# Optimization experiments

Hardware: AMD Instinct MI355X
Metric: run time of the kernel (lower is better)

The kernel has to match this reference:

```python
import jax, jax.numpy as jnp
import numpy as np
import math

B, D, T, R = 32, 512, 64, 49
K = 64
OUT = 1024


def setup_inputs() -> dict:
    key = jax.random.key(0)
    k_x, k_c, k_w = jax.random.split(key, 3)
    x = jax.random.normal(k_x, (B, D, T, R), dtype=jnp.float32)
    mask = jnp.ones((B, T), dtype=jnp.int32)
    centroids = jax.random.normal(k_c, (K, D), dtype=jnp.float32) / math.sqrt(D)
    conv_w = centroids  # reset_parameters() copies centroids into the 1x1 conv weight
    red_w = jax.random.normal(k_w, (OUT, K * D), dtype=jnp.float32) / math.sqrt(K * D)
    ln_gamma = jnp.ones((OUT,), dtype=jnp.float32)
    ln_beta = jnp.zeros((OUT,), dtype=jnp.float32)
    return {"x": x, "mask": mask, "centroids": centroids, "conv_w": conv_w,
            "red_w": red_w, "ln_gamma": ln_gamma, "ln_beta": ln_beta}


def _l2norm(v, axis):
    n = jnp.sqrt(jnp.sum(v * v, axis=axis, keepdims=True))
    return v / jnp.maximum(n, 1e-12)


def reference(x, mask, centroids, conv_w, red_w, ln_gamma, ln_beta):
    b, d, t, r = x.shape
    # 1x1 conv == contraction over channel dim: [b,k,t,r]
    logits = jnp.einsum('bdtr,kd->bktr', x, conv_w)
    assign = jax.nn.softmax(logits, axis=1)
    # mask applied to residual*assign == masking the assignments
    m = mask.astype(x.dtype)[:, None, :, None]          # [b,1,t,1]
    assign = assign * m
    a_sum = jnp.sum(assign, axis=(2, 3))                 # [b,k]
    # vlad[b,k,d] = sum_{t,r} a[b,k,t,r]*x[b,d,t,r] - a_sum[b,k]*c[k,d]
    vlad = jnp.einsum('bktr,bdtr->bkd', assign, x) - a_sum[:, :, None] * centroids[None]
    vlad = _l2norm(vlad, axis=2)                         # intra-normalization
    vlad = vlad.reshape(b, -1)                           # [b, K*D]
    vlad = _l2norm(vlad, axis=1)
    vlad = vlad @ red_w.T                                # [b, OUT]
    # LayerNorm (eps=1e-5)
    mu = jnp.mean(vlad, axis=-1, keepdims=True)
    var = jnp.mean((vlad - mu) ** 2, axis=-1, keepdims=True)
    return (vlad - mu) / jnp.sqrt(var + 1e-5) * ln_gamma + ln_beta
```

## Files before the change

kernel.cpp:

```cpp
#include <hip/hip_runtime.h>
#include <math.h>

#define BB 32
#define DD 512
#define TT 64
#define RR 49
#define TR 3136
#define KK 64
#define OUTN 1024
#define KD 32768
#define PSTR 1048576ull

typedef float f4 __attribute__((ext_vector_type(4)));
typedef short s8 __attribute__((ext_vector_type(8)));

#define OFF_ASSIGN 0ull
#define OFF_VLADP  12845056ull
#define OFF_VN     29622272ull
#define OFF_CWB    31719424ull
#define OFF_SS     31784960ull
#define OFF_ASUM   31793152ull
#define OFF_Y      31801344ull

__device__ __forceinline__ unsigned long long pack4(float a, float b, float c, float d) {
    union { float f; unsigned u; } A, B, C, D;
    A.f = a; B.f = b; C.f = c; D.f = d;
    unsigned lo = __builtin_amdgcn_perm(B.u + 0x8000u, A.u + 0x8000u, 0x07060302u);
    unsigned hi = __builtin_amdgcn_perm(D.u + 0x8000u, C.u + 0x8000u, 0x07060302u);
    return (unsigned long long)lo | ((unsigned long long)hi << 32);
}

__global__ __launch_bounds__(256) void kW(const float* __restrict__ convw,
                                          unsigned short* __restrict__ cwb) {
    int idx = blockIdx.x * 256 + threadIdx.x;
    f4 v = *(const f4*)(convw + idx * 4);
    *(unsigned long long*)(cwb + idx * 4) = pack4(v[0], v[1], v[2], v[3]);
}

__global__ __launch_bounds__(256) void kA(const float* __restrict__ x,
                                          const int* __restrict__ mask,
                                          const unsigned short* __restrict__ cwb,
                                          unsigned short* __restrict__ assign,
                                          float* __restrict__ asum) {
    __shared__ unsigned short xT_l[64 * 136];
    __shared__ float sm[64 * 68];
    __shared__ float redM[256], redS[256];

    const int blk = blockIdx.x;
    const int b = blk / 49;
    const int pc = blk % 49;
    const int p0 = pc * 64;
    const int tid = threadIdx.x;
    const int lane = tid & 63;
    const int wv = tid >> 6;
    const int quad = lane >> 4;
    const int l15 = lane & 15;

    f4 acc[4];
#pragma unroll
    for (int t = 0; t < 4; ++t) acc[t] = (f4){0.f, 0.f, 0.f, 0.f};

    const float* xb = x + (size_t)b * DD * TR;
    const unsigned short* cwrow = cwb + (wv * 16 + l15) * DD + quad * 8;

    for (int dc = 0; dc < 4; ++dc) {
        const int d0 = dc * 128;
        s8 af[4];
#pragma unroll
        for (int ks = 0; ks < 4; ++ks) af[ks] = *(const s8*)(cwrow + d0 + ks * 32);
        __syncthreads();
#pragma unroll
        for (int i = 0; i < 2; ++i) {
            int lin = i * 256 + tid;
            int dq = lin >> 4;
            int pq = lin & 15;
            const float* xp = xb + (size_t)(d0 + dq * 4) * TR + p0 + pq * 4;
            f4 a0 = *(const f4*)(xp);
            f4 a1 = *(const f4*)(xp + TR);
            f4 a2 = *(const f4*)(xp + 2 * TR);
            f4 a3 = *(const f4*)(xp + 3 * TR);
#pragma unroll
            for (int jj = 0; jj < 4; ++jj) {
                int j = (jj + pq) & 3;
                *(unsigned long long*)(xT_l + (pq * 4 + j) * 136 + dq * 4) =
                    pack4(a0[j], a1[j], a2[j], a3[j]);
            }
        }
        __syncthreads();
#pragma unroll
        for (int ks = 0; ks < 4; ++ks) {
            int off = ks * 32 + quad * 8;
#pragma unroll
            for (int t = 0; t < 4; ++t) {
                s8 bfr = *(const s8*)(xT_l + (t * 16 + l15) * 136 + off);
                acc[t] = __builtin_amdgcn_mfma_f32_16x16x32_bf16(af[ks], bfr, acc[t], 0, 0, 0);
            }
        }
    }
#pragma unroll
    for (int t = 0; t < 4; ++t)
#pragma unroll
        for (int r = 0; r < 4; ++r)
            sm[(wv * 16 + quad * 4 + r) * 68 + t * 16 + l15] = acc[t][r];
    __syncthreads();

    const int p = lane;
    float mx = -1e30f;
#pragma unroll
    for (int i = 0; i < 16; ++i) mx = fmaxf(mx, sm[(wv * 16 + i) * 68 + p]);
    redM[wv * 64 + p] = mx;
    __syncthreads();
    mx = fmaxf(fmaxf(redM[p], redM[64 + p]), fmaxf(redM[128 + p], redM[192 + p]));
    float s = 0.f;
#pragma unroll
    for (int i = 0; i < 16; ++i) {
        float e = __expf(sm[(wv * 16 + i) * 68 + p] - mx);
        sm[(wv * 16 + i) * 68 + p] = e;
        s += e;
    }
    redS[wv * 64 + p] = s;
    __syncthreads();
    float tot = redS[p] + redS[64 + p] + redS[128 + p] + redS[192 + p];
    const int tt = (p0 + p) / RR;
    const float inv = (float)mask[b * TT + tt] / tot;
#pragma unroll
    for (int i = 0; i < 16; ++i) {
        float v = sm[(wv * 16 + i) * 68 + p] * inv;
        sm[(wv * 16 + i) * 68 + p] = v;
        float r = v;
#pragma unroll
        for (int off = 32; off > 0; off >>= 1) r += __shfl_down(r, off, 64);
        if (lane == 0) atomicAdd(&asum[b * 64 + wv * 16 + i], r);
    }
    __syncthreads();
#pragma unroll
    for (int i = 0; i < 4; ++i) {
        int lin = i * 256 + tid;
        int kr = lin >> 4;
        int pqq = lin & 15;
        f4 v = *(const f4*)(sm + kr * 68 + pqq * 4);
        *(unsigned long long*)(assign + (size_t)(b * 64 + kr) * TR + p0 + pqq * 4) =
            pack4(v[0], v[1], v[2], v[3]);
    }
}

__global__ __launch_bounds__(256) void kB(const float* __restrict__ x,
                                          const unsigned short* __restrict__ assign,
                                          const float* __restrict__ asum,
                                          const float* __restrict__ cent,
                                          float* __restrict__ vladP) {
    __shared__ unsigned short as_l[64 * 72];
    __shared__ unsigned short x_l[64 * 72];

    const int blk = blockIdx.x;
    const int b  = blk >> 5;
    const int ds = (blk >> 2) & 7;
    const int ph = blk & 3;
    const int d0 = ds * 64;
    const int tid = threadIdx.x;
    const int lane = tid & 63;
    const int wv = tid >> 6;
    const int quad = lane >> 4;
    const int l15 = lane & 15;

    f4 acc[4];
#pragma unroll
    for (int t = 0; t < 4; ++t) acc[t] = (f4){0.f, 0.f, 0.f, 0.f};

    const int pcs = (ph * 49) >> 2;
    const int pce = ((ph + 1) * 49) >> 2;

    const int ar0 = tid >> 3, ac0 = tid & 7;
    const int xr0 = tid >> 4, xc0 = tid & 15;

    s8 asr[2];
    f4 xrr[4];
    auto LOADB = [&](int pc) {
        const int pp = pc * 64;
#pragma unroll
        for (int i = 0; i < 2; ++i)
            asr[i] = *(const s8*)(assign + (size_t)(b * 64 + ar0 + i * 32) * TR + pp + ac0 * 8);
#pragma unroll
        for (int i = 0; i < 4; ++i)
            xrr[i] = *(const f4*)(x + (size_t)(b * DD + d0 + xr0 + i * 16) * TR + pp + xc0 * 4);
    };
    auto STOREB = [&]() {
#pragma unroll
        for (int i = 0; i < 2; ++i)
            *(s8*)(as_l + (ar0 + i * 32) * 72 + ac0 * 8) = asr[i];
#pragma unroll
        for (int i = 0; i < 4; ++i)
            *(unsigned long long*)(x_l + (xr0 + i * 16) * 72 + xc0 * 4) =
                pack4(xrr[i][0], xrr[i][1], xrr[i][2], xrr[i][3]);
    };

    LOADB(pcs);
    for (int pc = pcs; pc < pce; ++pc) {
        __syncthreads();
        STOREB();
        if (pc + 1 < pce) LOADB(pc + 1);
        __syncthreads();
#pragma unroll
        for (int ks = 0; ks < 2; ++ks) {
            const int off = ks * 32 + quad * 8;
            s8 af = *(const s8*)(as_l + (wv * 16 + l15) * 72 + off);
#pragma unroll
            for (int t = 0; t < 4; ++t) {
                s8 bfr = *(const s8*)(x_l + (t * 16 + l15) * 72 + off);
                acc[t] = __builtin_amdgcn_mfma_f32_16x16x32_bf16(af, bfr, acc[t], 0, 0, 0);
            }
        }
    }
    float* vp = vladP + (size_t)ph * PSTR;
#pragma unroll
    for (int r = 0; r < 4; ++r) {
        const int k = wv * 16 + quad * 4 + r;
        float corr = (ph == 0) ? asum[b * 64 + k] : 0.f;
#pragma unroll
        for (int t = 0; t < 4; ++t) {
            const int d = d0 + t * 16 + l15;
            float v = acc[t][r];
            if (ph == 0) v -= corr * cent[k * DD + d];
            vp[(size_t)(b * 64 + k) * DD + d] = v;
        }
    }
}

__global__ __launch_bounds__(256) void kC1(const float* __restrict__ vladP,
                                           float* __restrict__ ss) {
    const int blk = blockIdx.x;
    const int b = blk >> 3;
    const int ks = blk & 7;
    const int tid = threadIdx.x;
    const int kr = tid >> 5;
    const int l32 = tid & 31;
    const int k = ks * 8 + kr;
    const float* q = vladP + (size_t)(b * 64 + k) * DD;
    float s = 0.f;
#pragma unroll
    for (int i = 0; i < 4; ++i) {
        f4 a0 = *(const f4*)(q + i * 128 + l32 * 4);
        f4 a1 = *(const f4*)(q + PSTR + i * 128 + l32 * 4);
        f4 a2 = *(const f4*)(q + 2 * PSTR + i * 128 + l32 * 4);
        f4 a3 = *(const f4*)(q + 3 * PSTR + i * 128 + l32 * 4);
#pragma unroll
        for (int j = 0; j < 4; ++j) {
            float v = (a0[j] + a1[j]) + (a2[j] + a3[j]);
            s = fmaf(v, v, s);
        }
    }
    for (int off = 16; off > 0; off >>= 1) s += __shfl_down(s, off, 32);
    if (l32 == 0) ss[b * 64 + k] = s;
}

__global__ __launch_bounds__(256) void kC2(const float* __restrict__ vladP,
                                           const float* __restrict__ ss,
                                           unsigned short* __restrict__ vn) {
    __shared__ float sc[64];
    const int blk = blockIdx.x;
    const int b = blk >> 3;
    const int js = blk & 7;
    const int tid = threadIdx.x;
    if (tid < 64) {
        float rn = sqrtf(ss[b * 64 + tid]);
        float inv = 1.f / fmaxf(rn, 1e-12f);
        float cb = rn * inv; cb = cb * cb;
        float g = cb;
        for (int off = 32; off > 0; off >>= 1) g += __shfl_down(g, off, 64);
        g = __shfl(g, 0, 64);
        float gi = 1.f / fmaxf(sqrtf(g), 1e-12f);
        sc[tid] = inv * gi;
    }
    __syncthreads();
    const float* q = vladP + (size_t)b * KD;
#pragma unroll
    for (int it = 0; it < 4; ++it) {
        int j = js * 4096 + it * 1024 + tid * 4;
        f4 a0 = *(const f4*)(q + j);
        f4 a1 = *(const f4*)(q + PSTR + j);
        f4 a2 = *(const f4*)(q + 2 * PSTR + j);
        f4 a3 = *(const f4*)(q + 3 * PSTR + j);
        float scl = sc[j >> 9];
        *(unsigned long long*)(vn + (size_t)b * KD + j) =
            pack4(((a0[0] + a1[0]) + (a2[0] + a3[0])) * scl,
                  ((a0[1] + a1[1]) + (a2[1] + a3[1])) * scl,
                  ((a0[2] + a1[2]) + (a2[2] + a3[2])) * scl,
                  ((a0[3] + a1[3]) + (a2[3] + a3[3])) * scl);
    }
}

__global__ __launch_bounds__(256) void kD(const unsigned short* __restrict__ vn,
                                          const float* __restrict__ redw,
                                          float* __restrict__ y) {
    __shared__ unsigned short rw_l[64 * 136];
    __shared__ unsigned short vl_l[32 * 136];

    const int blk = blockIdx.x;
    const int ot = blk & 15;
    const int js = blk >> 4;
    const int o0 = ot * 64;
    const int jb = js * 1024;
    const int tid = threadIdx.x;
    const int lane = tid & 63;
    const int wv = tid >> 6;
    const int quad = lane >> 4;
    const int l15 = lane & 15;

    f4 acc[2];
    acc[0] = (f4){0.f, 0.f, 0.f, 0.f};
    acc[1] = (f4){0.f, 0.f, 0.f, 0.f};

    const int rr0 = tid >> 5, rc0 = tid & 31;
    const int vr0 = tid >> 4, vc0 = tid & 15;
    f4 rwr[8];
    s8 vlr[2];
    auto LOADD = [&](int jc) {
        const int j0 = jb + jc * 128;
#pragma unroll
        for (int i = 0; i < 8; ++i)
            rwr[i] = *(const f4*)(redw + (size_t)(o0 + rr0 + i * 8) * KD + j0 + rc0 * 4);
#pragma unroll
        for (int i = 0; i < 2; ++i)
            vlr[i] = *(const s8*)(vn + (size_t)(vr0 + i * 16) * KD + j0 + vc0 * 8);
    };
    auto STORED = [&]() {
#pragma unroll
        for (int i = 0; i < 8; ++i)
            *(unsigned long long*)(rw_l + (rr0 + i * 8) * 136 + rc0 * 4) =
                pack4(rwr[i][0], rwr[i][1], rwr[i][2], rwr[i][3]);
#pragma unroll
        for (int i = 0; i < 2; ++i)
            *(s8*)(vl_l + (vr0 + i * 16) * 136 + vc0 * 8) = vlr[i];
    };

    LOADD(0);
    for (int jc = 0; jc < 8; ++jc) {
        __syncthreads();
        STORED();
        if (jc < 7) LOADD(jc + 1);
        __syncthreads();
#pragma unroll
        for (int ks = 0; ks < 4; ++ks) {
            const int off = ks * 32 + quad * 8;
            s8 bfr = *(const s8*)(rw_l + (wv * 16 + l15) * 136 + off);
#pragma unroll
            for (int t = 0; t < 2; ++t) {
                s8 af = *(const s8*)(vl_l + (t * 16 + l15) * 136 + off);
                acc[t] = __builtin_amdgcn_mfma_f32_16x16x32_bf16(af, bfr, acc[t], 0, 0, 0);
            }
        }
    }
#pragma unroll
    for (int t = 0; t < 2; ++t)
#pragma unroll
        for (int r = 0; r < 4; ++r) {
            int bq = t * 16 + quad * 4 + r;
            int o = o0 + wv * 16 + l15;
            atomicAdd(&y[(size_t)bq * OUTN + o], acc[t][r]);
        }
}

__global__ __launch_bounds__(256) void kE(const float* __restrict__ y,
                                          const float* __restrict__ gamma,
                                          const float* __restrict__ beta,
                                          float* __restrict__ out) {
    __shared__ float s1s[4], s2s[4];
    __shared__ float mu_s, rstd_s;

    const int b = blockIdx.x;
    const int tid = threadIdx.x;
    const int wave = tid >> 6;
    const int lane = tid & 63;

    f4 v = *(const f4*)(y + (size_t)b * OUTN + tid * 4);
    float s1 = v[0] + v[1] + v[2] + v[3];
    float s2 = v[0] * v[0] + v[1] * v[1] + v[2] * v[2] + v[3] * v[3];
    for (int off = 32; off > 0; off >>= 1) {
        s1 += __shfl_down(s1, off, 64);
        s2 += __shfl_down(s2, off, 64);
    }
    if (lane == 0) { s1s[wave] = s1; s2s[wave] = s2; }
    __syncthreads();
    if (tid == 0) {
        float S1 = s1s[0] + s1s[1] + s1s[2] + s1s[3];
        float S2 = s2s[0] + s2s[1] + s2s[2] + s2s[3];
        float mu = S1 / (float)OUTN;
        float var = S2 / (float)OUTN - mu * mu;
        mu_s = mu;
        rstd_s = 1.0f / sqrtf(var + 1e-5f);
    }
    __syncthreads();
    const float mu = mu_s, rstd = rstd_s;
    f4 g = *(const f4*)(gamma + tid * 4);
    f4 be = *(const f4*)(beta + tid * 4);
    f4 o;
#pragma unroll
    for (int i = 0; i < 4; ++i) o[i] = (v[i] - mu) * rstd * g[i] + be[i];
    *(f4*)(out + (size_t)b * OUTN + tid * 4) = o;
}

extern "C" void kernel_launch(void* const* d_in, const int* in_sizes, int n_in,
                              void* d_out, int out_size, void* d_ws, size_t ws_size,
                              hipStream_t stream) {
    const float* x     = (const float*)d_in[0];
    const int*   mask  = (const int*)d_in[1];
    const float* cent  = (const float*)d_in[2];
    const float* convw = (const float*)d_in[3];
    const float* redw  = (const float*)d_in[4];
    const float* gam   = (const float*)d_in[5];
    const float* bet   = (const float*)d_in[6];
    float* out = (float*)d_out;
    char* w = (char*)d_ws;

    unsigned short* assign = (unsigned short*)(w + OFF_ASSIGN);
    float*          vladP  = (float*)(w + OFF_VLADP);
    unsigned short* vn     = (unsigned short*)(w + OFF_VN);
    unsigned short* cwb    = (unsigned short*)(w + OFF_CWB);
    float*          ss     = (float*)(w + OFF_SS);
    float*          asum   = (float*)(w + OFF_ASUM);
    float*          y      = (float*)(w + OFF_Y);

    hipMemsetAsync(asum, 0, 64 * BB * sizeof(float), stream);
    hipMemsetAsync(y, 0, BB * OUTN * sizeof(float), stream);

    kW<<<32, 256, 0, stream>>>(convw, cwb);
    kA<<<BB * 49, 256, 0, stream>>>(x, mask, cwb, assign, asum);
    kB<<<BB * 8 * 4, 256, 0, stream>>>(x, assign, asum, cent, vladP);
    kC1<<<BB * 8, 256, 0, stream>>>(vladP, ss);
    kC2<<<BB * 8, 256, 0, stream>>>(vladP, ss, vn);
    kD<<<16 * 32, 256, 0, stream>>>(vn, redw, y);
    kE<<<BB, 256, 0, stream>>>(y, gam, bet, out);
}
```

Measured before the change: 446.6 us.

## Double-buffer x tiles in assignment kernel, widen kB/kD split across blocks

The assignment kernel now double-buffers the transposed x tile in shared memory, loading the next 128-channel chunk from global while MFMAs run on the current one. The softmax scratch reuses the first buffer. The aggregation kernel splits positions into 6 partial sums instead of 4, with a launch-bounds occupancy hint, and the reduction GEMM splits K into 64 chunks instead of 32. These give more blocks and overlap, at the cost of more partial-sum traffic in kC1/kC2 and more atomics in kD.

Result: no change. 453.8 us (+1.6%).

```diff
diff --git a/kernel.cpp b/kernel.cpp
--- a/kernel.cpp
+++ b/kernel.cpp
@@ -10,17 +10,18 @@
 #define OUTN 1024
 #define KD 32768
 #define PSTR 1048576ull
+#define NPH 6
 
 typedef float f4 __attribute__((ext_vector_type(4)));
 typedef short s8 __attribute__((ext_vector_type(8)));
 
 #define OFF_ASSIGN 0ull
 #define OFF_VLADP  12845056ull
-#define OFF_VN     29622272ull
-#define OFF_CWB    31719424ull
-#define OFF_SS     31784960ull
-#define OFF_ASUM   31793152ull
-#define OFF_Y      31801344ull
+#define OFF_VN     38010880ull
+#define OFF_CWB    40108032ull
+#define OFF_SS     40173568ull
+#define OFF_ASUM   40181760ull
+#define OFF_Y      40189952ull
 
 __device__ __forceinline__ unsigned long long pack4(float a, float b, float c, float d) {
     union { float f; unsigned u; } A, B, C, D;
@@ -42,9 +43,10 @@
                                           const unsigned short* __restrict__ cwb,
                                           unsigned short* __restrict__ assign,
                                           float* __restrict__ asum) {
-    __shared__ unsigned short xT_l[64 * 136];
-    __shared__ float sm[64 * 68];
+    __shared__ unsigned short xT0[64 * 136];
+    __shared__ unsigned short xT1[64 * 136];
     __shared__ float redM[256], redS[256];
+    float* sm = (float*)xT0;
 
     const int blk = blockIdx.x;
     const int b = blk / 49;
@@ -55,48 +57,67 @@
     const int wv = tid >> 6;
     const int quad = lane >> 4;
     const int l15 = lane & 15;
+    const int pq = tid & 15;
+    const int dq0 = tid >> 4;
 
     f4 acc[4];
 #pragma unroll
     for (int t = 0; t < 4; ++t) acc[t] = (f4){0.f, 0.f, 0.f, 0.f};
 
-    const float* xb = x + (size_t)b * DD * TR;
+    const float* xb = x + (size_t)b * DD * TR + p0 + pq * 4;
     const unsigned short* cwrow = cwb + (wv * 16 + l15) * DD + quad * 8;
 
+    f4 g00, g01, g02, g03;
+    f4 g10, g11, g12, g13;
+
+#define KA_XLOAD(D0)                                                          \
+    {                                                                         \
+        const float* xp0 = xb + (size_t)((D0) + dq0 * 4) * TR;                \
+        const float* xp1 = xb + (size_t)((D0) + (dq0 + 16) * 4) * TR;         \
+        g00 = *(const f4*)(xp0);          g01 = *(const f4*)(xp0 + TR);       \
+        g02 = *(const f4*)(xp0 + 2 * TR); g03 = *(const f4*)(xp0 + 3 * TR);   \
+        g10 = *(const f4*)(xp1);          g11 = *(const f4*)(xp1 + TR);       \
+        g12 = *(const f4*)(xp1 + 2 * TR); g13 = *(const f4*)(xp1 + 3 * TR);   \
+    }
+
+#define KA_XST1(BUF, JJ)                                                      \
+    {                                                                         \
+        int j = ((JJ) + pq) & 3;               \
+        *(unsigned long long*)((BUF) + (pq * 4 + j) * 136 + dq0 * 4) =        \
+            pack4(g00[j], g01[j], g02[j], g03[j]);                            \
+        *(unsigned long long*)((BUF) + (pq * 4 + j) * 136 + (dq0 + 16) * 4) = \
+            pack4(g10[j], g11[j], g12[j], g13[j]);                            \
+    }
+#define KA_XSTORE(BUF) { KA_XST1(BUF, 0) KA_XST1(BUF, 1) KA_XST1(BUF, 2) KA_XST1(BUF, 3) }
+
+    KA_XLOAD(0);
+    KA_XSTORE(xT0);
+    KA_XLOAD(128);
+    __syncthreads();
+
+#pragma unroll
     for (int dc = 0; dc < 4; ++dc) {
-        const int d0 = dc * 128;
+        unsigned short* cur = (dc & 1) ? xT1 : xT0;
+        unsigned short* nxt = (dc & 1) ? xT0 : xT1;
+        if (dc < 3) KA_XSTORE(nxt);
+        if (dc < 2) KA_XLOAD((dc + 2) * 128);
         s8 af[4];
-#pragma unroll
-        for (int ks = 0; ks < 4; ++ks) af[ks] = *(const s8*)(cwrow + d0 + ks * 32);
-        __syncthreads();
-#pragma unroll
-        for (int i = 0; i < 2; ++i) {
-            int lin = i * 256 + tid;
-            int dq = lin >> 4;
-            int pq = lin & 15;
-            const float* xp = xb + (size_t)(d0 + dq * 4) * TR + p0 + pq * 4;
-            f4 a0 = *(const f4*)(xp);
-            f4 a1 = *(const f4*)(xp + TR);
-            f4 a2 = *(const f4*)(xp + 2 * TR);
-            f4 a3 = *(const f4*)(xp + 3 * TR);
-#pragma unroll
-            for (int jj = 0; jj < 4; ++jj) {
-                int j = (jj + pq) & 3;
-                *(unsigned long long*)(xT_l + (pq * 4 + j) * 136 + dq * 4) =
-                    pack4(a0[j], a1[j], a2[j], a3[j]);
-            }
-        }
-        __syncthreads();
+        af[0] = *(const s8*)(cwrow + dc * 128);
+        af[1] = *(const s8*)(cwrow + dc * 128 + 32);
+        af[2] = *(const s8*)(cwrow + dc * 128 + 64);
+        af[3] = *(const s8*)(cwrow + dc * 128 + 96);
 #pragma unroll
         for (int ks = 0; ks < 4; ++ks) {
             int off = ks * 32 + quad * 8;
 #pragma unroll
             for (int t = 0; t < 4; ++t) {
-                s8 bfr = *(const s8*)(xT_l + (t * 16 + l15) * 136 + off);
+                s8 bfr = *(const s8*)(cur + (t * 16 + l15) * 136 + off);
                 acc[t] = __builtin_amdgcn_mfma_f32_16x16x32_bf16(af[ks], bfr, acc[t], 0, 0, 0);
             }
         }
-    }
+        __syncthreads();
+    }
+
 #pragma unroll
     for (int t = 0; t < 4; ++t)
 #pragma unroll
@@ -144,18 +165,19 @@
     }
 }
 
-__global__ __launch_bounds__(256) void kB(const float* __restrict__ x,
-                                          const unsigned short* __restrict__ assign,
-                                          const float* __restrict__ asum,
-                                          const float* __restrict__ cent,
-                                          float* __restrict__ vladP) {
+__global__ __launch_bounds__(256, 6) void kB(const float* __restrict__ x,
+                                             const unsigned short* __restrict__ assign,
+                                             const float* __restrict__ asum,
+                                             const float* __restrict__ cent,
+                                             float* __restrict__ vladP) {
     __shared__ unsigned short as_l[64 * 72];
     __shared__ unsigned short x_l[64 * 72];
 
     const int blk = blockIdx.x;
-    const int b  = blk >> 5;
-    const int ds = (blk >> 2) & 7;
-    const int ph = blk & 3;
+    const int b   = blk / 48;
+    const int rem = blk % 48;
+    const int ds  = rem / NPH;
+    const int ph  = rem % NPH;
     const int d0 = ds * 64;
     const int tid = threadIdx.x;
     const int lane = tid & 63;
@@ -167,8 +189,8 @@
 #pragma unroll
     for (int t = 0; t < 4; ++t) acc[t] = (f4){0.f, 0.f, 0.f, 0.f};
 
-    const int pcs = (ph * 49) >> 2;
-    const int pce = ((ph + 1) * 49) >> 2;
+    const int pcs = (ph * 49) / NPH;
+    const int pce = ((ph + 1) * 49) / NPH;
 
     const int ar0 = tid >> 3, ac0 = tid & 7;
     const int xr0 = tid >> 4, xc0 = tid & 15;
@@ -239,15 +261,14 @@
     float s = 0.f;
 #pragma unroll
     for (int i = 0; i < 4; ++i) {
-        f4 a0 = *(const f4*)(q + i * 128 + l32 * 4);
-        f4 a1 = *(const f4*)(q + PSTR + i * 128 + l32 * 4);
-        f4 a2 = *(const f4*)(q + 2 * PSTR + i * 128 + l32 * 4);
-        f4 a3 = *(const f4*)(q + 3 * PSTR + i * 128 + l32 * 4);
-#pragma unroll
-        for (int j = 0; j < 4; ++j) {
-            float v = (a0[j] + a1[j]) + (a2[j] + a3[j]);
-            s = fmaf(v, v, s);
-        }
+        f4 v = *(const f4*)(q + i * 128 + l32 * 4);
+#pragma unroll
+        for (int pp = 1; pp < NPH; ++pp) {
+            f4 a = *(const f4*)(q + pp * PSTR + i * 128 + l32 * 4);
+            v[0] += a[0]; v[1] += a[1]; v[2] += a[2]; v[3] += a[3];
+        }
+#pragma unroll
+        for (int j = 0; j < 4; ++j) s = fmaf(v[j], v[j], s);
     }
     for (int off = 16; off > 0; off >>= 1) s += __shfl_down(s, off, 32);
     if (l32 == 0) ss[b * 64 + k] = s;
@@ -276,16 +297,15 @@
 #pragma unroll
     for (int it = 0; it < 4; ++it) {
         int j = js * 4096 + it * 1024 + tid * 4;
-        f4 a0 = *(const f4*)(q + j);
-        f4 a1 = *(const f4*)(q + PSTR + j);
-        f4 a2 = *(const f4*)(q + 2 * PSTR + j);
-        f4 a3 = *(const f4*)(q + 3 * PSTR + j);
+        f4 v = *(const f4*)(q + j);
+#pragma unroll
+        for (int pp = 1; pp < NPH; ++pp) {
+            f4 a = *(const f4*)(q + pp * PSTR + j);
+            v[0] += a[0]; v[1] += a[1]; v[2] += a[2]; v[3] += a[3];
+        }
         float scl = sc[j >> 9];
         *(unsigned long long*)(vn + (size_t)b * KD + j) =
-            pack4(((a0[0] + a1[0]) + (a2[0] + a3[0])) * scl,
-                  ((a0[1] + a1[1]) + (a2[1] + a3[1])) * scl,
-                  ((a0[2] + a1[2]) + (a2[2] + a3[2])) * scl,
-                  ((a0[3] + a1[3]) + (a2[3] + a3[3])) * scl);
+            pack4(v[0] * scl, v[1] * scl, v[2] * scl, v[3] * scl);
     }
 }
 
@@ -299,7 +319,7 @@
     const int ot = blk & 15;
     const int js = blk >> 4;
     const int o0 = ot * 64;
-    const int jb = js * 1024;
+    const int jb = js * 512;
     const int tid = threadIdx.x;
     const int lane = tid & 63;
     const int wv = tid >> 6;
@@ -334,10 +354,10 @@
     };
 
     LOADD(0);
-    for (int jc = 0; jc < 8; ++jc) {
+    for (int jc = 0; jc < 4; ++jc) {
         __syncthreads();
         STORED();
-        if (jc < 7) LOADD(jc + 1);
+        if (jc < 3) LOADD(jc + 1);
         __syncthreads();
 #pragma unroll
         for (int ks = 0; ks < 4; ++ks) {
@@ -425,9 +445,9 @@
 
     kW<<<32, 256, 0, stream>>>(convw, cwb);
     kA<<<BB * 49, 256, 0, stream>>>(x, mask, cwb, assign, asum);
-    kB<<<BB * 8 * 4, 256, 0, stream>>>(x, assign, asum, cent, vladP);
+    kB<<<BB * 8 * NPH, 256, 0, stream>>>(x, assign, asum, cent, vladP);
     kC1<<<BB * 8, 256, 0, stream>>>(vladP, ss);
     kC2<<<BB * 8, 256, 0, stream>>>(vladP, ss, vn);
-    kD<<<16 * 32, 256, 0, stream>>>(vn, redw, y);
+    kD<<<16 * 64, 256, 0, stream>>>(vn, redw, y);
     kE<<<BB, 256, 0, stream>>>(y, gam, bet, out);
 }
```
